# Kernel tuning notes

Measured on AMD Instinct MI355X. Metric: run time of the kernel, lower is better.

The kernel has to match this reference:

```python
import jax, jax.numpy as jnp
import numpy as np

N_NODES = 100000
N_GRAPHS = 128
NEG_SLOPE = 0.2


def _param(key, shape, scale=0.1):
    return jax.random.normal(key, shape, dtype=jnp.float32) * scale


def setup_inputs() -> dict:
    key = jax.random.key(0)
    ks = jax.random.split(key, 16)
    E = 1600000
    IN, H, C, OUT = 128, 2, 64, 10
    x = jax.random.normal(ks[0], (N_NODES, IN), dtype=jnp.float32)
    edge_index = jax.random.randint(ks[1], (2, E), 0, N_NODES, dtype=jnp.int64)
    batch = jnp.sort(jax.random.randint(ks[2], (N_NODES,), 0, N_GRAPHS, dtype=jnp.int64))
    return {
        "x": x,
        "W1": _param(ks[3], (IN, H * C)),
        "att_src1": _param(ks[4], (H, C)),
        "att_dst1": _param(ks[5], (H, C)),
        "b1": jnp.zeros((C,), jnp.float32),
        "W2": _param(ks[6], (C, H * C)),
        "att_src2": _param(ks[7], (H, C)),
        "att_dst2": _param(ks[8], (H, C)),
        "b2": jnp.zeros((C,), jnp.float32),
        "Wfc": _param(ks[9], (C, OUT)),
        "bfc": jnp.zeros((OUT,), jnp.float32),
        "edge_index": edge_index,
        "batch": batch,
    }


def gat_conv(x, src, dst, W, att_src, att_dst, bias):
    # x: [N, Fin]; W: [Fin, H*C]; att_*: [H, C]; PyG GATConv, concat=False
    H, C = att_src.shape
    xw = (x @ W).reshape(-1, H, C)                       # [N, H, C]
    a_src = jnp.einsum('nhc,hc->nh', xw, att_src)        # [N, H]
    a_dst = jnp.einsum('nhc,hc->nh', xw, att_dst)        # [N, H]
    logits = a_src[src] + a_dst[dst]                     # [E, H]
    logits = jax.nn.leaky_relu(logits, NEG_SLOPE)
    # segment softmax over edges sharing the same dst node
    m = jax.ops.segment_max(logits, dst, num_segments=N_NODES)   # [N, H]
    e = jnp.exp(logits - m[dst])
    s = jax.ops.segment_sum(e, dst, num_segments=N_NODES)        # [N, H]
    alpha = e / (s[dst] + 1e-16)                         # [E, H]
    out = jax.ops.segment_sum(alpha[:, :, None] * xw[src], dst, num_segments=N_NODES)
    return out.mean(axis=1) + bias                       # concat=False -> mean over heads


def reference(x, W1, att_src1, att_dst1, b1, W2, att_src2, att_dst2, b2, Wfc, bfc, edge_index, batch):
    loop = jnp.arange(N_NODES, dtype=edge_index.dtype)   # add_self_loops=True
    src = jnp.concatenate([edge_index[0], loop])
    dst = jnp.concatenate([edge_index[1], loop])
    h = jax.nn.relu(gat_conv(x, src, dst, W1, att_src1, att_dst1, b1))
    h = jax.nn.relu(gat_conv(h, src, dst, W2, att_src2, att_dst2, b2))
    g = jax.ops.segment_sum(h, batch, num_segments=N_GRAPHS)     # global_add_pool
    logits = g @ Wfc + bfc
    return jax.nn.log_softmax(logits, axis=1)
```

## Files before the change

### kernel.cpp

```cpp
#include <hip/hip_runtime.h>
#include <cstdint>
#include <cstddef>

#define NNODES 100000
#define NGRAPHS 128
#define NEG_SLOPE 0.2f
#define MAXDEG 64

typedef __attribute__((ext_vector_type(8))) short short8;
typedef __attribute__((ext_vector_type(4))) float f32x4;

static __device__ __forceinline__ unsigned int bf16_rne(float f) {
    unsigned int x = __float_as_uint(f);
    return (x + 0x7fffu + ((x >> 16) & 1u)) >> 16;
}

__global__ void prep_w_kernel(const float* __restrict__ W1, const float* __restrict__ W2,
                              unsigned short* __restrict__ wt1, unsigned short* __restrict__ wt2) {
    int idx = blockIdx.x * 256 + threadIdx.x;
    if (idx < 128 * 128) {
        int c = idx & 127, k = idx >> 7;
        wt1[c * 128 + k] = (unsigned short)bf16_rne(W1[k * 128 + c]);
    } else {
        int j = idx - 128 * 128;
        if (j < 128 * 64) {
            int c = j & 127, k = j >> 7;
            wt2[c * 64 + k] = (unsigned short)bf16_rne(W2[k * 128 + c]);
        }
    }
}

template <int K, bool BF16IN>
__global__ __launch_bounds__(256) void gemm_mfma_kernel(
        const void* __restrict__ Av, const unsigned short* __restrict__ Wt,
        unsigned short* __restrict__ xwp16,
        const float* __restrict__ att_src, const float* __restrict__ att_dst,
        float* __restrict__ asrc, float* __restrict__ adst, int M) {
    constexpr int BST = K + 8;
    __shared__ __align__(16) unsigned short B_lds[128 * BST];
    int tid = threadIdx.x;
    int row0 = blockIdx.x * 64;

    constexpr int K8 = K / 8;
    #pragma unroll
    for (int i = 0; i < 128 * K8 / 256; ++i) {
        int idx = tid + i * 256;
        int c = idx / K8, k8 = idx % K8;
        *(short8*)&B_lds[c * BST + k8 * 8] = *(const short8*)&Wt[c * K + k8 * 8];
    }
    __syncthreads();

    int w = tid >> 6, l = tid & 63;
    int lr = l & 15, lg = l >> 4;
    int row = row0 + 16 * w + lr;
    bool rv = row < M;

    short8 afr[K / 32];
    if constexpr (BF16IN) {
        const unsigned short* A = (const unsigned short*)Av;
        #pragma unroll
        for (int ks = 0; ks < K / 32; ++ks) {
            short8 v = {};
            if (rv) v = *(const short8*)&A[(size_t)row * K + lg * 8 + ks * 32];
            afr[ks] = v;
        }
    } else {
        const float* A = (const float*)Av;
        #pragma unroll
        for (int ks = 0; ks < K / 32; ++ks) {
            short8 v = {};
            if (rv) {
                float4 f0 = *(const float4*)&A[(size_t)row * K + lg * 8 + ks * 32];
                float4 f1 = *(const float4*)&A[(size_t)row * K + lg * 8 + ks * 32 + 4];
                v[0] = (short)bf16_rne(f0.x); v[1] = (short)bf16_rne(f0.y);
                v[2] = (short)bf16_rne(f0.z); v[3] = (short)bf16_rne(f0.w);
                v[4] = (short)bf16_rne(f1.x); v[5] = (short)bf16_rne(f1.y);
                v[6] = (short)bf16_rne(f1.z); v[7] = (short)bf16_rne(f1.w);
            }
            afr[ks] = v;
        }
    }

    f32x4 acc[8] = {};
    #pragma unroll
    for (int ks = 0; ks < K / 32; ++ks) {
        #pragma unroll
        for (int t = 0; t < 8; ++t) {
            short8 b = *(const short8*)&B_lds[(16 * t + lr) * BST + lg * 8 + ks * 32];
            acc[t] = __builtin_amdgcn_mfma_f32_16x16x32_bf16(afr[ks], b, acc[t], 0, 0, 0);
        }
    }

    float ps0[4] = {}, pd0[4] = {}, ps1[4] = {}, pd1[4] = {};
    #pragma unroll
    for (int t = 0; t < 8; ++t) {
        int c = 16 * t + lr;
        int h = t >> 2;
        int cc = c & 63;
        float ws = att_src[h * 64 + cc];
        float wd = att_dst[h * 64 + cc];
        #pragma unroll
        for (int r = 0; r < 4; ++r) {
            int orow = row0 + 16 * w + lg * 4 + r;
            float v = acc[t][r];
            if (h == 0) { ps0[r] += v * ws; pd0[r] += v * wd; }
            else        { ps1[r] += v * ws; pd1[r] += v * wd; }
            if (orow < M) xwp16[(size_t)orow * 128 + cc * 2 + h] = (unsigned short)bf16_rne(v);
        }
    }
    #pragma unroll
    for (int off = 1; off < 16; off <<= 1) {
        #pragma unroll
        for (int r = 0; r < 4; ++r) {
            ps0[r] += __shfl_xor(ps0[r], off);
            pd0[r] += __shfl_xor(pd0[r], off);
            ps1[r] += __shfl_xor(ps1[r], off);
            pd1[r] += __shfl_xor(pd1[r], off);
        }
    }
    if (lr == 0) {
        #pragma unroll
        for (int r = 0; r < 4; ++r) {
            int orow = row0 + 16 * w + lg * 4 + r;
            if (orow < M) {
                asrc[orow * 2 + 0] = ps0[r]; adst[orow * 2 + 0] = pd0[r];
                asrc[orow * 2 + 1] = ps1[r]; adst[orow * 2 + 1] = pd1[r];
            }
        }
    }
}

__global__ void scatter_kernel(const int* __restrict__ src, const int* __restrict__ dst,
                               int* __restrict__ cursor, int* __restrict__ esrc, int E, int ET) {
    int e = blockIdx.x * blockDim.x + threadIdx.x;
    if (e >= ET) return;
    int s = (e < E) ? src[e] : (e - E);
    int d = (e < E) ? dst[e] : (e - E);
    int slot = atomicAdd(&cursor[d], 1);
    esrc[(size_t)d * MAXDEG + slot] = s;
}

template <bool TO_G>
__global__ __launch_bounds__(64) void aggregate_kernel(
        const int* __restrict__ deg, const int* __restrict__ esrc,
        const float2* __restrict__ asrc2, const float2* __restrict__ adst2,
        const unsigned int* __restrict__ xwp, const float* __restrict__ bias,
        unsigned short* __restrict__ outb, const int* __restrict__ batch,
        float* __restrict__ g) {
    int lane = threadIdx.x;
    int n = blockIdx.x;
    int row = n * MAXDEG, dg = deg[n];
    float2 ad = adst2[n];
    float acc0 = 0.f, acc1 = 0.f, s0 = 0.f, s1 = 0.f;
    int i = 0;

#define LOADG(k) int sn##k = __builtin_nontemporal_load(&esrc[row + i + k]); \
                 float2 a##k = asrc2[sn##k]; \
                 unsigned int u##k = xwp[(size_t)sn##k * 64 + lane]
#define FMAG(k)  { float l0 = a##k.x + ad.x; float l1 = a##k.y + ad.y; \
                   l0 = fmaxf(l0, NEG_SLOPE * l0); l1 = fmaxf(l1, NEG_SLOPE * l1); \
                   float e0 = __expf(l0), e1 = __expf(l1); \
                   s0 += e0; s1 += e1; \
                   acc0 += e0 * __uint_as_float(u##k << 16); \
                   acc1 += e1 * __uint_as_float(u##k & 0xffff0000u); }

    for (; i + 8 <= dg; i += 8) {
        LOADG(0); LOADG(1); LOADG(2); LOADG(3);
        LOADG(4); LOADG(5); LOADG(6); LOADG(7);
        FMAG(0); FMAG(1); FMAG(2); FMAG(3);
        FMAG(4); FMAG(5); FMAG(6); FMAG(7);
    }
    for (; i + 2 <= dg; i += 2) {
        LOADG(0); LOADG(1);
        FMAG(0); FMAG(1);
    }
    if (i < dg) {
        LOADG(0);
        FMAG(0);
    }
#undef LOADG
#undef FMAG

    float v = 0.5f * (acc0 / (s0 + 1e-16f) + acc1 / (s1 + 1e-16f)) + bias[lane];
    v = (v > 0.f) ? v : 0.f;
    if (TO_G) atomicAdd(&g[batch[n] * 64 + lane], v);
    else outb[(size_t)n * 64 + lane] = (unsigned short)bf16_rne(v);
}

__global__ void final_fc_kernel(const float* __restrict__ g, const float* __restrict__ Wfc,
                                const float* __restrict__ bfc, float* __restrict__ out) {
    int gi = threadIdx.x;
    if (gi >= NGRAPHS) return;
    float logit[10];
    #pragma unroll
    for (int o = 0; o < 10; ++o) logit[o] = bfc[o];
    for (int c = 0; c < 64; ++c) {
        float gv = g[gi * 64 + c];
        #pragma unroll
        for (int o = 0; o < 10; ++o) logit[o] += gv * Wfc[c * 10 + o];
    }
    float mx = logit[0];
    #pragma unroll
    for (int o = 1; o < 10; ++o) mx = fmaxf(mx, logit[o]);
    float se = 0.f;
    #pragma unroll
    for (int o = 0; o < 10; ++o) se += expf(logit[o] - mx);
    float lse = mx + logf(se);
    #pragma unroll
    for (int o = 0; o < 10; ++o) out[gi * 10 + o] = logit[o] - lse;
}

extern "C" void kernel_launch(void* const* d_in, const int* in_sizes, int n_in,
                              void* d_out, int out_size, void* d_ws, size_t ws_size,
                              hipStream_t stream) {
    const float* x        = (const float*)d_in[0];
    const float* W1       = (const float*)d_in[1];
    const float* att_src1 = (const float*)d_in[2];
    const float* att_dst1 = (const float*)d_in[3];
    const float* b1       = (const float*)d_in[4];
    const float* W2       = (const float*)d_in[5];
    const float* att_src2 = (const float*)d_in[6];
    const float* att_dst2 = (const float*)d_in[7];
    const float* b2       = (const float*)d_in[8];
    const float* Wfc      = (const float*)d_in[9];
    const float* bfc      = (const float*)d_in[10];
    const int*   eidx     = (const int*)d_in[11];
    const int*   batch    = (const int*)d_in[12];
    float* out = (float*)d_out;

    const int E  = in_sizes[11] / 2;
    const int ET = E + NNODES;
    const int* srcp = eidx;
    const int* dstp = eidx + E;

    char* w = (char*)d_ws;
    unsigned int* xwp = (unsigned int*)w;    w += (size_t)NNODES * 64 * 4;
    float* asrc = (float*)w;                 w += (size_t)NNODES * 2 * 4;
    float* adst = (float*)w;                 w += (size_t)NNODES * 2 * 4;
    unsigned short* h1 = (unsigned short*)w; w += (size_t)NNODES * 64 * 2;
    int* cursor  = (int*)w;                  w += (size_t)NNODES * 4;
    float* g    = (float*)w;                 w += (size_t)NGRAPHS * 64 * 4;
    int* esrc    = (int*)w;                  w += (size_t)NNODES * MAXDEG * 4;
    unsigned short* wt1 = (unsigned short*)w; w += (size_t)128 * 128 * 2;
    unsigned short* wt2 = (unsigned short*)w; w += (size_t)128 * 64 * 2;

    const int BLK = 256;
    int grid_et   = (ET + BLK - 1) / BLK;

    hipMemsetAsync(cursor, 0, ((size_t)NNODES + NGRAPHS * 64) * 4, stream);

    scatter_kernel<<<grid_et, BLK, 0, stream>>>(srcp, dstp, cursor, esrc, E, ET);
    prep_w_kernel<<<(128 * 192 + 255) / 256, 256, 0, stream>>>(W1, W2, wt1, wt2);

    int gemm_grid = (NNODES + 63) / 64;

    gemm_mfma_kernel<128, false><<<gemm_grid, BLK, 0, stream>>>(x, wt1, (unsigned short*)xwp,
                                                                att_src1, att_dst1, asrc, adst, NNODES);
    aggregate_kernel<false><<<NNODES, 64, 0, stream>>>(cursor, esrc,
                                                       (const float2*)asrc, (const float2*)adst,
                                                       xwp, b1, h1, nullptr, nullptr);

    gemm_mfma_kernel<64, true><<<gemm_grid, BLK, 0, stream>>>(h1, wt2, (unsigned short*)xwp,
                                                              att_src2, att_dst2, asrc, adst, NNODES);
    aggregate_kernel<true><<<NNODES, 64, 0, stream>>>(cursor, esrc,
                                                      (const float2*)asrc, (const float2*)adst,
                                                      xwp, b2, nullptr, batch, g);

    final_fc_kernel<<<1, 128, 0, stream>>>(g, Wfc, bfc, out);
}
```

Before: 369.1 us.

## Fuse edge scatter with first GEMM, handle self-loops in aggregate, drop LDS staging

Merges the edge-scatter kernel and the first GEMM into a single launch, with block IDs split between the two roles so the scatter atomics overlap the MFMA work. Self-loop edges are no longer written to the adjacency buffer; the aggregate kernel seeds its accumulators with the node's own term instead. The GEMMs now read the weight tile straight from global memory, with no LDS staging and barrier, and scatter writes use nontemporal stores. This saves a launch and the self-loop atomics, but adds redundant global/L2 weight reads per wave and could shift the degree cap if any node's edge count depended on the self-loop slot.

New measurement: 447.2 us. +21.1%, slower.

```diff
diff --git a/kernel.cpp b/kernel.cpp
--- a/kernel.cpp
+++ b/kernel.cpp
@@ -31,25 +31,12 @@
 }
 
 template <int K, bool BF16IN>
-__global__ __launch_bounds__(256) void gemm_mfma_kernel(
-        const void* __restrict__ Av, const unsigned short* __restrict__ Wt,
+static __device__ __forceinline__ void gemm_body(
+        int bx, int tid, const void* __restrict__ Av, const unsigned short* __restrict__ Wt,
         unsigned short* __restrict__ xwp16,
         const float* __restrict__ att_src, const float* __restrict__ att_dst,
         float* __restrict__ asrc, float* __restrict__ adst, int M) {
-    constexpr int BST = K + 8;
-    __shared__ __align__(16) unsigned short B_lds[128 * BST];
-    int tid = threadIdx.x;
-    int row0 = blockIdx.x * 64;
-
-    constexpr int K8 = K / 8;
-    #pragma unroll
-    for (int i = 0; i < 128 * K8 / 256; ++i) {
-        int idx = tid + i * 256;
-        int c = idx / K8, k8 = idx % K8;
-        *(short8*)&B_lds[c * BST + k8 * 8] = *(const short8*)&Wt[c * K + k8 * 8];
-    }
-    __syncthreads();
-
+    int row0 = bx * 64;
     int w = tid >> 6, l = tid & 63;
     int lr = l & 15, lg = l >> 4;
     int row = row0 + 16 * w + lr;
@@ -86,7 +73,7 @@
     for (int ks = 0; ks < K / 32; ++ks) {
         #pragma unroll
         for (int t = 0; t < 8; ++t) {
-            short8 b = *(const short8*)&B_lds[(16 * t + lr) * BST + lg * 8 + ks * 32];
+            short8 b = *(const short8*)&Wt[(size_t)(16 * t + lr) * K + lg * 8 + ks * 32];
             acc[t] = __builtin_amdgcn_mfma_f32_16x16x32_bf16(afr[ks], b, acc[t], 0, 0, 0);
         }
     }
@@ -130,14 +117,33 @@
     }
 }
 
-__global__ void scatter_kernel(const int* __restrict__ src, const int* __restrict__ dst,
-                               int* __restrict__ cursor, int* __restrict__ esrc, int E, int ET) {
-    int e = blockIdx.x * blockDim.x + threadIdx.x;
-    if (e >= ET) return;
-    int s = (e < E) ? src[e] : (e - E);
-    int d = (e < E) ? dst[e] : (e - E);
-    int slot = atomicAdd(&cursor[d], 1);
-    esrc[(size_t)d * MAXDEG + slot] = s;
+__global__ __launch_bounds__(256) void fused_scatter_gemm1_kernel(
+        const int* __restrict__ src, const int* __restrict__ dst,
+        int* __restrict__ cursor, int* __restrict__ esrc, int E, int nscat,
+        const float* __restrict__ A, const unsigned short* __restrict__ Wt,
+        unsigned short* __restrict__ xwp16,
+        const float* __restrict__ att_src, const float* __restrict__ att_dst,
+        float* __restrict__ asrc, float* __restrict__ adst, int M) {
+    if ((int)blockIdx.x < nscat) {
+        int e = blockIdx.x * 256 + threadIdx.x;
+        if (e < E) {
+            int s = src[e], d = dst[e];
+            int slot = atomicAdd(&cursor[d], 1);
+            __builtin_nontemporal_store(s, &esrc[(size_t)d * MAXDEG + slot]);
+        }
+        return;
+    }
+    gemm_body<128, false>(blockIdx.x - nscat, threadIdx.x, A, Wt, xwp16,
+                          att_src, att_dst, asrc, adst, M);
+}
+
+__global__ __launch_bounds__(256) void gemm2_kernel(
+        const unsigned short* __restrict__ A, const unsigned short* __restrict__ Wt,
+        unsigned short* __restrict__ xwp16,
+        const float* __restrict__ att_src, const float* __restrict__ att_dst,
+        float* __restrict__ asrc, float* __restrict__ adst, int M) {
+    gemm_body<64, true>(blockIdx.x, threadIdx.x, A, Wt, xwp16,
+                        att_src, att_dst, asrc, adst, M);
 }
 
 template <bool TO_G>
@@ -151,7 +157,17 @@
     int n = blockIdx.x;
     int row = n * MAXDEG, dg = deg[n];
     float2 ad = adst2[n];
-    float acc0 = 0.f, acc1 = 0.f, s0 = 0.f, s1 = 0.f;
+    float acc0, acc1, s0, s1;
+    {
+        float2 a = asrc2[n];
+        unsigned int u = xwp[(size_t)n * 64 + lane];
+        float l0 = a.x + ad.x, l1 = a.y + ad.y;
+        l0 = fmaxf(l0, NEG_SLOPE * l0); l1 = fmaxf(l1, NEG_SLOPE * l1);
+        float e0 = __expf(l0), e1 = __expf(l1);
+        s0 = e0; s1 = e1;
+        acc0 = e0 * __uint_as_float(u << 16);
+        acc1 = e1 * __uint_as_float(u & 0xffff0000u);
+    }
     int i = 0;
 
 #define LOADG(k) int sn##k = __builtin_nontemporal_load(&esrc[row + i + k]); \
@@ -229,7 +245,6 @@
     float* out = (float*)d_out;
 
     const int E  = in_sizes[11] / 2;
-    const int ET = E + NNODES;
     const int* srcp = eidx;
     const int* dstp = eidx + E;
 
@@ -245,23 +260,23 @@
     unsigned short* wt2 = (unsigned short*)w; w += (size_t)128 * 64 * 2;
 
     const int BLK = 256;
-    int grid_et   = (ET + BLK - 1) / BLK;
+    int nscat = (E + BLK - 1) / BLK;
+    int gemm_grid = (NNODES + 63) / 64;
 
     hipMemsetAsync(cursor, 0, ((size_t)NNODES + NGRAPHS * 64) * 4, stream);
 
-    scatter_kernel<<<grid_et, BLK, 0, stream>>>(srcp, dstp, cursor, esrc, E, ET);
     prep_w_kernel<<<(128 * 192 + 255) / 256, 256, 0, stream>>>(W1, W2, wt1, wt2);
 
-    int gemm_grid = (NNODES + 63) / 64;
-
-    gemm_mfma_kernel<128, false><<<gemm_grid, BLK, 0, stream>>>(x, wt1, (unsigned short*)xwp,
-                                                                att_src1, att_dst1, asrc, adst, NNODES);
+    fused_scatter_gemm1_kernel<<<nscat + gemm_grid, BLK, 0, stream>>>(
+        srcp, dstp, cursor, esrc, E, nscat,
+        x, wt1, (unsigned short*)xwp, att_src1, att_dst1, asrc, adst, NNODES);
+
     aggregate_kernel<false><<<NNODES, 64, 0, stream>>>(cursor, esrc,
                                                        (const float2*)asrc, (const float2*)adst,
                                                        xwp, b1, h1, nullptr, nullptr);
 
-    gemm_mfma_kernel<64, true><<<gemm_grid, BLK, 0, stream>>>(h1, wt2, (unsigned short*)xwp,
-                                                              att_src2, att_dst2, asrc, adst, NNODES);
+    gemm2_kernel<<<gemm_grid, BLK, 0, stream>>>(h1, wt2, (unsigned short*)xwp,
+                                                att_src2, att_dst2, asrc, adst, NNODES);
     aggregate_kernel<true><<<NNODES, 64, 0, stream>>>(cursor, esrc,
                                                       (const float2*)asrc, (const float2*)adst,
                                                       xwp, b2, nullptr, batch, g);
```
